# Optimization experiments

Hardware: AMD Instinct MI355X
Metric: run time of the kernel (lower is better)

Reference implementation:

```python
import jax, jax.numpy as jnp
import numpy as np

L, N = 200, 256  # event_list_length, num_nodes


def setup_inputs() -> dict:
    key = jax.random.key(0)
    ks = jax.random.split(key, 7)
    time = jax.random.uniform(ks[0], (2,), dtype=jnp.float32)
    event_list = jax.random.normal(ks[1], (L + 1, N, N), dtype=jnp.float32)
    u_begin = jax.random.uniform(ks[2], (N, N, 3), dtype=jnp.float32)
    # xavier-ish scales for params
    a = jax.random.normal(ks[3], (L, N, N, 3), dtype=jnp.float32) * 0.05
    w = jax.random.normal(ks[4], (L, N, 1, N), dtype=jnp.float32) * 0.05
    liner_w = jax.random.normal(ks[5], (N, 3), dtype=jnp.float32) * 0.5
    liner_b = jax.random.normal(ks[6], (N,), dtype=jnp.float32) * 0.1
    return {"time": time, "event_list": event_list, "u_begin": u_begin,
            "a": a, "w": w, "liner_w": liner_w, "liner_b": liner_b,
            "batch_size": 2}


def reference(time, event_list, u_begin, a, w, liner_w, liner_b, batch_size):
    # event_list[:-1]; consumed in pairs (start, start+1) with batch_size == 2
    T = event_list.shape[0] - 1
    S = T // batch_size                      # number of scan steps
    n = event_list.shape[1]
    e2 = event_list[:T].reshape(S, 2, n, n)          # [S,2,N,N]
    a2 = a[:T].reshape(S, 2, n, n, 3)                # [S,2,N,N,3]
    w2 = w[:T, :, 0, :].reshape(S, 2, n, n)          # [S,2,N,N] (squeeze the 1-dim)
    t0, t1 = time[0], time[1]                        # original always uses time[0], time[1]

    def step(u, xs):
        ep, ap, wp = xs                              # [2,N,N], [2,N,N,3], [2,N,N]
        # per-node scalar dot: w[start][node] @ event_begin[k][node]
        dot0 = jnp.einsum('nk,nk->n', wp[0], ep[0])  # [N]
        dot1 = jnp.einsum('nk,nk->n', wp[1], ep[1])
        # math.exp in the original returns a Python float -> constant w.r.t. autograd
        f0 = jax.lax.stop_gradient(jnp.exp(-dot0 * t0))[:, None, None]
        f1 = jax.lax.stop_gradient(jnp.exp(-dot1 * t1))[:, None, None]
        lamda = u + ap[0] * f0 + ap[1] * f1          # [N,N,3]
        temp = jax.nn.softmax(lamda, axis=-1)        # softmax over the 3-dim (dim=1 of [N,3] per node)
        # per-node Linear(3,1): temp[node] @ W_node^T + b_node -> [N,N]
        out = jnp.einsum('nmc,nc->nm', temp, liner_w) + liner_b[:, None]
        # state update was .detach().cpu().numpy() -> stop_gradient
        return jax.lax.stop_gradient(temp), out

    _, outs = jax.lax.scan(step, u_begin, (e2, a2, w2))
    return outs                                      # [S, N, N] == [T/2, N, N]
```

## Files before the change

### kernel.cpp

```cpp
#include <hip/hip_runtime.h>


#define NN    256
#define TT    200
#define SS    100
#define DRING 6

__global__ __launch_bounds__(256) void f_kernel(
    const float* __restrict__ timep,
    const float* __restrict__ ev,
    const float* __restrict__ w,
    float* __restrict__ fws)
{
    const int tid  = threadIdx.x;
    const int lane = tid & 63;
    const int row  = blockIdx.x * 4 + (tid >> 6);
    const int t    = row >> 8;
    const int n    = row & 255;

    const size_t off = (size_t)t * (NN * NN) + (size_t)n * NN;
    const float4 wv  = ((const float4*)(w  + off))[lane];
    const float4 evv = ((const float4*)(ev + off))[lane];

    float d = wv.x * evv.x;
    d = fmaf(wv.y, evv.y, d);
    d = fmaf(wv.z, evv.z, d);
    d = fmaf(wv.w, evv.w, d);
#pragma unroll
    for (int o = 1; o < 64; o <<= 1) d += __shfl_xor(d, o, 64);

    if (lane == 0) {
        const float tsel = (t & 1) ? timep[1] : timep[0];
        fws[n * TT + t] = __expf(-d * tsel);
    }
}

__global__ __launch_bounds__(256) void scan_kernel(
    const float* __restrict__ fws,
    const float* __restrict__ ub,
    const float* __restrict__ a,
    const float* __restrict__ lw,
    const float* __restrict__ lb,
    float* __restrict__ out)
{
    __shared__ float stg[DRING][4][768];
    __shared__ float fsl[TT];

    const int n    = blockIdx.x;
    const int tid  = threadIdx.x;
    const int lane = tid & 63;
    const int wv   = tid >> 6;

    if (tid < TT) fsl[tid] = fws[n * TT + tid];

    const size_t cb = (size_t)n * (NN * 3) + (size_t)tid * 3;
    float u0 = ub[cb + 0], u1 = ub[cb + 1], u2 = ub[cb + 2];
    const float w0 = lw[n * 3 + 0];
    const float w1 = lw[n * 3 + 1];
    const float w2 = lw[n * 3 + 2];
    const float bb = lb[n];

    const int m3 = tid * 3;
    float* op = out + (size_t)n * NN + tid;

    __syncthreads();

    const float* abase = a + (size_t)n * (NN * 3) + (size_t)lane * 4;

#define STAGE(qq, bidx)                                                        \
    do {                                                                       \
        const float* gp_ = abase + (size_t)(4 * (qq) + wv) * ((size_t)NN * NN * 3); \
        float* lp_ = &stg[bidx][wv][0];                                        \
        __builtin_amdgcn_global_load_lds(                                      \
            (const __attribute__((address_space(1))) void*)gp_,                \
            (__attribute__((address_space(3))) void*)lp_, 16, 0, 0);           \
        __builtin_amdgcn_global_load_lds(                                      \
            (const __attribute__((address_space(1))) void*)(gp_ + 256),        \
            (__attribute__((address_space(3))) void*)(lp_ + 256), 16, 0, 0);   \
        __builtin_amdgcn_global_load_lds(                                      \
            (const __attribute__((address_space(1))) void*)(gp_ + 512),        \
            (__attribute__((address_space(3))) void*)(lp_ + 512), 16, 0, 0);   \
    } while (0)

    STAGE(0, 0); STAGE(1, 1); STAGE(2, 2); STAGE(3, 3); STAGE(4, 4);

#define STEPX(BI, SA, SB, FA, FB, SOUT)                                        \
    do {                                                                       \
        float l0 = fmaf(stg[BI][SA][m3 + 0], FA, fmaf(stg[BI][SB][m3 + 0], FB, u0)); \
        float l1 = fmaf(stg[BI][SA][m3 + 1], FA, fmaf(stg[BI][SB][m3 + 1], FB, u1)); \
        float l2 = fmaf(stg[BI][SA][m3 + 2], FA, fmaf(stg[BI][SB][m3 + 2], FB, u2)); \
        float mx = fmaxf(l0, fmaxf(l1, l2));                                   \
        float e0 = __expf(l0 - mx), e1 = __expf(l1 - mx), e2 = __expf(l2 - mx);\
        float iv = __builtin_amdgcn_rcpf(e0 + e1 + e2);                        \
        u0 = e0 * iv; u1 = e1 * iv; u2 = e2 * iv;                              \
        __builtin_nontemporal_store(fmaf(u0, w0, fmaf(u1, w1, fmaf(u2, w2, bb))), \
                                    op + (size_t)(SOUT) * (NN * NN));          \
    } while (0)

#define PHASE(GG, VN, DOSTAGE, BI)                                             \
    do {                                                                       \
        asm volatile("s_waitcnt vmcnt(" #VN ")" ::: "memory");                 \
        __builtin_amdgcn_s_barrier();                                          \
        asm volatile("" ::: "memory");                                         \
        if (DOSTAGE) {                                                         \
            const int bs_ = (BI) ? (BI) - 1 : (DRING - 1);                     \
            STAGE((GG) + DRING - 1, bs_);                                      \
        }                                                                      \
        asm volatile("" ::: "memory");                                         \
        const float fa0 = fsl[4 * (GG) + 0], fb0 = fsl[4 * (GG) + 1];          \
        STEPX(BI, 0, 1, fa0, fb0, 2 * (GG));                                   \
        const float fa1 = fsl[4 * (GG) + 2], fb1 = fsl[4 * (GG) + 3];          \
        STEPX(BI, 2, 3, fa1, fb1, 2 * (GG) + 1);                               \
    } while (0)

    PHASE(0, 12, 1, 0);
    PHASE(1, 14, 1, 1);
    PHASE(2, 16, 1, 2);
    PHASE(3, 18, 1, 3);
    PHASE(4, 20, 1, 4);
    {
        int b = 5;
        for (int g = 5; g <= 44; ++g) {
            PHASE(g, 22, 1, b);
            b = (b == DRING - 1) ? 0 : b + 1;
        }
    }
    PHASE(45, 22, 0, 3);
    PHASE(46, 19, 0, 4);
    PHASE(47, 16, 0, 5);
    PHASE(48, 13, 0, 0);
    PHASE(49, 10, 0, 1);

#undef PHASE
#undef STEPX
#undef STAGE
}

extern "C" void kernel_launch(void* const* d_in, const int* in_sizes, int n_in,
                              void* d_out, int out_size, void* d_ws, size_t ws_size,
                              hipStream_t stream) {
    const float* timep = (const float*)d_in[0];
    const float* ev    = (const float*)d_in[1];
    const float* ub    = (const float*)d_in[2];
    const float* a     = (const float*)d_in[3];
    const float* w     = (const float*)d_in[4];
    const float* lw    = (const float*)d_in[5];
    const float* lb    = (const float*)d_in[6];
    float* out = (float*)d_out;
    float* fws = (float*)d_ws;

    f_kernel<<<(TT * NN) / 4, 256, 0, stream>>>(timep, ev, w, fws);
    scan_kernel<<<NN, 256, 0, stream>>>(fws, ub, a, lw, lb, out);
}
```

Measured before the change: 308.0 us.

## Fuse decay-factor computation into scan kernel and deepen LDS prefetch ring

Removes the separate f_kernel and computes each node's 200 exp-decay factors inside the scan block, writing them straight to shared memory while the first a-tiles are already being prefetched. This drops one launch and the workspace round trip. The async LDS ring grows from 6 to 8 stages, with vmcnt thresholds adjusted to match. The cost is that only 256 blocks now do the dot-product work serially inside the scan kernel, and more LDS is used per block.

```diff
diff --git a/kernel.cpp b/kernel.cpp
--- a/kernel.cpp
+++ b/kernel.cpp
@@ -4,41 +4,14 @@
 #define NN    256
 #define TT    200
 #define SS    100
-#define DRING 6
+#define DRING 8
 
-__global__ __launch_bounds__(256) void f_kernel(
+__global__ __launch_bounds__(256) void fused_kernel(
     const float* __restrict__ timep,
     const float* __restrict__ ev,
-    const float* __restrict__ w,
-    float* __restrict__ fws)
-{
-    const int tid  = threadIdx.x;
-    const int lane = tid & 63;
-    const int row  = blockIdx.x * 4 + (tid >> 6);
-    const int t    = row >> 8;
-    const int n    = row & 255;
-
-    const size_t off = (size_t)t * (NN * NN) + (size_t)n * NN;
-    const float4 wv  = ((const float4*)(w  + off))[lane];
-    const float4 evv = ((const float4*)(ev + off))[lane];
-
-    float d = wv.x * evv.x;
-    d = fmaf(wv.y, evv.y, d);
-    d = fmaf(wv.z, evv.z, d);
-    d = fmaf(wv.w, evv.w, d);
-#pragma unroll
-    for (int o = 1; o < 64; o <<= 1) d += __shfl_xor(d, o, 64);
-
-    if (lane == 0) {
-        const float tsel = (t & 1) ? timep[1] : timep[0];
-        fws[n * TT + t] = __expf(-d * tsel);
-    }
-}
-
-__global__ __launch_bounds__(256) void scan_kernel(
-    const float* __restrict__ fws,
     const float* __restrict__ ub,
     const float* __restrict__ a,
+    const float* __restrict__ w,
     const float* __restrict__ lw,
     const float* __restrict__ lb,
     float* __restrict__ out)
@@ -50,20 +23,6 @@
     const int tid  = threadIdx.x;
     const int lane = tid & 63;
     const int wv   = tid >> 6;
-
-    if (tid < TT) fsl[tid] = fws[n * TT + tid];
-
-    const size_t cb = (size_t)n * (NN * 3) + (size_t)tid * 3;
-    float u0 = ub[cb + 0], u1 = ub[cb + 1], u2 = ub[cb + 2];
-    const float w0 = lw[n * 3 + 0];
-    const float w1 = lw[n * 3 + 1];
-    const float w2 = lw[n * 3 + 2];
-    const float bb = lb[n];
-
-    const int m3 = tid * 3;
-    float* op = out + (size_t)n * NN + tid;
-
-    __syncthreads();
 
     const float* abase = a + (size_t)n * (NN * 3) + (size_t)lane * 4;
 
@@ -82,7 +41,52 @@
             (__attribute__((address_space(3))) void*)(lp_ + 512), 16, 0, 0);   \
     } while (0)
 
-    STAGE(0, 0); STAGE(1, 1); STAGE(2, 2); STAGE(3, 3); STAGE(4, 4);
+    STAGE(0, 0); STAGE(1, 1); STAGE(2, 2); STAGE(3, 3);
+    STAGE(4, 4); STAGE(5, 5); STAGE(6, 6);
+
+    {
+        const float t0 = timep[0];
+        const float t1 = timep[1];
+        const float tsel = (wv & 1) ? t1 : t0;
+        const size_t rowoff = (size_t)n * NN;
+        const float* wrow = w  + rowoff;
+        const float* erow = ev + rowoff;
+        for (int t = wv; t < TT; t += 20) {
+            float d[5];
+#pragma unroll
+            for (int q = 0; q < 5; ++q) {
+                const int tq = t + 4 * q;
+                float4 wvv = ((const float4*)(wrow + (size_t)tq * (NN * NN)))[lane];
+                float4 evv = ((const float4*)(erow + (size_t)tq * (NN * NN)))[lane];
+                float dq = wvv.x * evv.x;
+                dq = fmaf(wvv.y, evv.y, dq);
+                dq = fmaf(wvv.z, evv.z, dq);
+                dq = fmaf(wvv.w, evv.w, dq);
+                d[q] = dq;
+            }
+#pragma unroll
+            for (int o = 1; o < 64; o <<= 1) {
+#pragma unroll
+                for (int q = 0; q < 5; ++q) d[q] += __shfl_xor(d[q], o, 64);
+            }
+            if (lane == 0) {
+#pragma unroll
+                for (int q = 0; q < 5; ++q)
+                    fsl[t + 4 * q] = __expf(-d[q] * tsel);
+            }
+        }
+    }
+
+    const size_t cb = (size_t)n * (NN * 3) + (size_t)tid * 3;
+    float u0 = ub[cb + 0], u1 = ub[cb + 1], u2 = ub[cb + 2];
+    const float w0 = lw[n * 3 + 0];
+    const float w1 = lw[n * 3 + 1];
+    const float w2 = lw[n * 3 + 2];
+    const float bb = lb[n];
+    const int m3 = tid * 3;
+    float* op = out + (size_t)n * NN + tid;
+
+    __syncthreads();
 
 #define STEPX(BI, SA, SB, FA, FB, SOUT)                                        \
     do {                                                                       \
@@ -100,36 +104,40 @@
 #define PHASE(GG, VN, DOSTAGE, BI)                                             \
     do {                                                                       \
         asm volatile("s_waitcnt vmcnt(" #VN ")" ::: "memory");                 \
+        __builtin_amdgcn_sched_barrier(0);                                     \
         __builtin_amdgcn_s_barrier();                                          \
-        asm volatile("" ::: "memory");                                         \
         if (DOSTAGE) {                                                         \
             const int bs_ = (BI) ? (BI) - 1 : (DRING - 1);                     \
             STAGE((GG) + DRING - 1, bs_);                                      \
         }                                                                      \
-        asm volatile("" ::: "memory");                                         \
+        __builtin_amdgcn_sched_barrier(0);                                     \
         const float fa0 = fsl[4 * (GG) + 0], fb0 = fsl[4 * (GG) + 1];          \
         STEPX(BI, 0, 1, fa0, fb0, 2 * (GG));                                   \
         const float fa1 = fsl[4 * (GG) + 2], fb1 = fsl[4 * (GG) + 3];          \
         STEPX(BI, 2, 3, fa1, fb1, 2 * (GG) + 1);                               \
     } while (0)
 
-    PHASE(0, 12, 1, 0);
-    PHASE(1, 14, 1, 1);
-    PHASE(2, 16, 1, 2);
-    PHASE(3, 18, 1, 3);
-    PHASE(4, 20, 1, 4);
+    PHASE(0, 18, 1, 0);
+    PHASE(1, 20, 1, 1);
+    PHASE(2, 22, 1, 2);
+    PHASE(3, 24, 1, 3);
+    PHASE(4, 26, 1, 4);
+    PHASE(5, 28, 1, 5);
+    PHASE(6, 30, 1, 6);
     {
-        int b = 5;
-        for (int g = 5; g <= 44; ++g) {
-            PHASE(g, 22, 1, b);
-            b = (b == DRING - 1) ? 0 : b + 1;
+        int b = 7;
+        for (int g = 7; g <= 42; ++g) {
+            PHASE(g, 32, 1, b);
+            b = (b + 1) & 7;
         }
     }
-    PHASE(45, 22, 0, 3);
-    PHASE(46, 19, 0, 4);
-    PHASE(47, 16, 0, 5);
-    PHASE(48, 13, 0, 0);
-    PHASE(49, 10, 0, 1);
+    PHASE(43, 32, 0, 3);
+    PHASE(44, 29, 0, 4);
+    PHASE(45, 26, 0, 5);
+    PHASE(46, 23, 0, 6);
+    PHASE(47, 20, 0, 7);
+    PHASE(48, 17, 0, 0);
+    PHASE(49, 14, 0, 1);
 
 #undef PHASE
 #undef STEPX
@@ -147,8 +155,6 @@
     const float* lw    = (const float*)d_in[5];
     const float* lb    = (const float*)d_in[6];
     float* out = (float*)d_out;
-    float* fws = (float*)d_ws;
 
-    f_kernel<<<(TT * NN) / 4, 256, 0, stream>>>(timep, ev, w, fws);
-    scan_kernel<<<NN, 256, 0, stream>>>(fws, ub, a, lw, lb, out);
+    fused_kernel<<<NN, 256, 0, stream>>>(timep, ev, ub, a, w, lw, lb, out);
 }
```

New measurement: 309.3 us. No clear change (+0.4%).

## Fuse exponent-factor kernel into scan kernel with register prefetch ring

Applied to the files above, without the earlier changes.

Merges the per-row dot/exp kernel into the scan kernel, so each block computes its own node's decay factors in chunks, interleaved with the scan steps. This removes the second launch and the workspace round trip. The LDS staging ring for `a` is replaced by a per-thread register ring of eight steps loaded directly from global memory. In exchange, each block now also streams the w and ev rows for its node, and it adds more barriers and register pressure.

```diff
diff --git a/kernel.cpp b/kernel.cpp
--- a/kernel.cpp
+++ b/kernel.cpp
@@ -1,139 +1,160 @@
 #include <hip/hip_runtime.h>
 
 
-#define NN    256
-#define TT    200
-#define SS    100
-#define DRING 6
+#define NN 256
+#define TT 200
+#define SS 100
+#define RD 8
 
-__global__ __launch_bounds__(256) void f_kernel(
+__global__ __launch_bounds__(256) void fused_kernel(
     const float* __restrict__ timep,
     const float* __restrict__ ev,
-    const float* __restrict__ w,
-    float* __restrict__ fws)
-{
-    const int tid  = threadIdx.x;
-    const int lane = tid & 63;
-    const int row  = blockIdx.x * 4 + (tid >> 6);
-    const int t    = row >> 8;
-    const int n    = row & 255;
-
-    const size_t off = (size_t)t * (NN * NN) + (size_t)n * NN;
-    const float4 wv  = ((const float4*)(w  + off))[lane];
-    const float4 evv = ((const float4*)(ev + off))[lane];
-
-    float d = wv.x * evv.x;
-    d = fmaf(wv.y, evv.y, d);
-    d = fmaf(wv.z, evv.z, d);
-    d = fmaf(wv.w, evv.w, d);
-#pragma unroll
-    for (int o = 1; o < 64; o <<= 1) d += __shfl_xor(d, o, 64);
-
-    if (lane == 0) {
-        const float tsel = (t & 1) ? timep[1] : timep[0];
-        fws[n * TT + t] = __expf(-d * tsel);
-    }
-}
-
-__global__ __launch_bounds__(256) void scan_kernel(
-    const float* __restrict__ fws,
     const float* __restrict__ ub,
     const float* __restrict__ a,
+    const float* __restrict__ w,
     const float* __restrict__ lw,
     const float* __restrict__ lb,
     float* __restrict__ out)
 {
-    __shared__ float stg[DRING][4][768];
-    __shared__ float fsl[TT];
+    __shared__ float2 fs2[SS];
 
     const int n    = blockIdx.x;
     const int tid  = threadIdx.x;
     const int lane = tid & 63;
     const int wv   = tid >> 6;
 
-    if (tid < TT) fsl[tid] = fws[n * TT + tid];
+    const float tm0 = timep[0];
+    const float tm1 = timep[1];
 
+    const float* wrow = w  + (size_t)n * NN;
+    const float* erow = ev + (size_t)n * NN;
+
+    float4 wA, eA, wB, eB, wC, eC, wD, eD;
+
+#define LOADROWS(WX, EX, WY, EY, TB)                                           \
+    do {                                                                       \
+        const size_t r0_ = (size_t)(TB) * (NN * NN);                           \
+        WX = ((const float4*)(wrow + r0_))[lane];                              \
+        EX = ((const float4*)(erow + r0_))[lane];                              \
+        WY = ((const float4*)(wrow + r0_ + NN * NN))[lane];                    \
+        EY = ((const float4*)(erow + r0_ + NN * NN))[lane];                    \
+    } while (0)
+
+    LOADROWS(wA, eA, wB, eB, 2 * wv);
+
+    const size_t TS = (size_t)NN * NN * 3;
     const size_t cb = (size_t)n * (NN * 3) + (size_t)tid * 3;
+    const float* ab = a + cb;
+    float rg[RD][6];
+#pragma unroll
+    for (int j = 0; j < RD; ++j) {
+        const float* p_ = ab + (size_t)(2 * j) * TS;
+        rg[j][0] = p_[0];      rg[j][1] = p_[1];      rg[j][2] = p_[2];
+        rg[j][3] = p_[TS + 0]; rg[j][4] = p_[TS + 1]; rg[j][5] = p_[TS + 2];
+    }
+
     float u0 = ub[cb + 0], u1 = ub[cb + 1], u2 = ub[cb + 2];
     const float w0 = lw[n * 3 + 0];
     const float w1 = lw[n * 3 + 1];
     const float w2 = lw[n * 3 + 2];
     const float bb = lb[n];
-
-    const int m3 = tid * 3;
     float* op = out + (size_t)n * NN + tid;
 
-    __syncthreads();
-
-    const float* abase = a + (size_t)n * (NN * 3) + (size_t)lane * 4;
-
-#define STAGE(qq, bidx)                                                        \
+#define REDUCE(WX, EX, WY, EY, Q)                                              \
     do {                                                                       \
-        const float* gp_ = abase + (size_t)(4 * (qq) + wv) * ((size_t)NN * NN * 3); \
-        float* lp_ = &stg[bidx][wv][0];                                        \
-        __builtin_amdgcn_global_load_lds(                                      \
-            (const __attribute__((address_space(1))) void*)gp_,                \
-            (__attribute__((address_space(3))) void*)lp_, 16, 0, 0);           \
-        __builtin_amdgcn_global_load_lds(                                      \
-            (const __attribute__((address_space(1))) void*)(gp_ + 256),        \
-            (__attribute__((address_space(3))) void*)(lp_ + 256), 16, 0, 0);   \
-        __builtin_amdgcn_global_load_lds(                                      \
-            (const __attribute__((address_space(1))) void*)(gp_ + 512),        \
-            (__attribute__((address_space(3))) void*)(lp_ + 512), 16, 0, 0);   \
+        float d0_ = WX.x * EX.x;                                               \
+        d0_ = fmaf(WX.y, EX.y, d0_);                                           \
+        d0_ = fmaf(WX.z, EX.z, d0_);                                           \
+        d0_ = fmaf(WX.w, EX.w, d0_);                                           \
+        float d1_ = WY.x * EY.x;                                               \
+        d1_ = fmaf(WY.y, EY.y, d1_);                                           \
+        d1_ = fmaf(WY.z, EY.z, d1_);                                           \
+        d1_ = fmaf(WY.w, EY.w, d1_);                                           \
+        _Pragma("unroll")                                                      \
+        for (int o_ = 1; o_ < 64; o_ <<= 1) {                                  \
+            d0_ += __shfl_xor(d0_, o_, 64);                                    \
+            d1_ += __shfl_xor(d1_, o_, 64);                                    \
+        }                                                                      \
+        if (lane == 0)                                                         \
+            fs2[4 * (Q) + wv] =                                                \
+                make_float2(__expf(-d0_ * tm0), __expf(-d1_ * tm1));           \
     } while (0)
 
-    STAGE(0, 0); STAGE(1, 1); STAGE(2, 2); STAGE(3, 3); STAGE(4, 4);
-
-#define STEPX(BI, SA, SB, FA, FB, SOUT)                                        \
+#define FENCE_BAR                                                              \
     do {                                                                       \
-        float l0 = fmaf(stg[BI][SA][m3 + 0], FA, fmaf(stg[BI][SB][m3 + 0], FB, u0)); \
-        float l1 = fmaf(stg[BI][SA][m3 + 1], FA, fmaf(stg[BI][SB][m3 + 1], FB, u1)); \
-        float l2 = fmaf(stg[BI][SA][m3 + 2], FA, fmaf(stg[BI][SB][m3 + 2], FB, u2)); \
-        float mx = fmaxf(l0, fmaxf(l1, l2));                                   \
-        float e0 = __expf(l0 - mx), e1 = __expf(l1 - mx), e2 = __expf(l2 - mx);\
-        float iv = __builtin_amdgcn_rcpf(e0 + e1 + e2);                        \
-        u0 = e0 * iv; u1 = e1 * iv; u2 = e2 * iv;                              \
-        __builtin_nontemporal_store(fmaf(u0, w0, fmaf(u1, w1, fmaf(u2, w2, bb))), \
-                                    op + (size_t)(SOUT) * (NN * NN));          \
+        asm volatile("s_waitcnt lgkmcnt(0)" ::: "memory");                     \
+        __builtin_amdgcn_s_barrier();                                          \
+        __builtin_amdgcn_sched_barrier(0);                                     \
     } while (0)
 
-#define PHASE(GG, VN, DOSTAGE, BI)                                             \
+#define STEP(S, J, RF)                                                         \
     do {                                                                       \
-        asm volatile("s_waitcnt vmcnt(" #VN ")" ::: "memory");                 \
-        __builtin_amdgcn_s_barrier();                                          \
-        asm volatile("" ::: "memory");                                         \
-        if (DOSTAGE) {                                                         \
-            const int bs_ = (BI) ? (BI) - 1 : (DRING - 1);                     \
-            STAGE((GG) + DRING - 1, bs_);                                      \
+        const float2 ff_ = fs2[(S)];                                           \
+        float l0_ = fmaf(rg[J][0], ff_.x, fmaf(rg[J][3], ff_.y, u0));          \
+        float l1_ = fmaf(rg[J][1], ff_.x, fmaf(rg[J][4], ff_.y, u1));          \
+        float l2_ = fmaf(rg[J][2], ff_.x, fmaf(rg[J][5], ff_.y, u2));          \
+        if (RF) {           \
+            const float* pR_ = ab + (size_t)(2 * ((S) + RD)) * TS;             \
+            rg[J][0] = pR_[0];                                                 \
+            rg[J][1] = pR_[1];                                                 \
+            rg[J][2] = pR_[2];                                                 \
+            rg[J][3] = pR_[TS + 0];                                            \
+            rg[J][4] = pR_[TS + 1];                                            \
+            rg[J][5] = pR_[TS + 2];                                            \
         }                                                                      \
-        asm volatile("" ::: "memory");                                         \
-        const float fa0 = fsl[4 * (GG) + 0], fb0 = fsl[4 * (GG) + 1];          \
-        STEPX(BI, 0, 1, fa0, fb0, 2 * (GG));                                   \
-        const float fa1 = fsl[4 * (GG) + 2], fb1 = fsl[4 * (GG) + 3];          \
-        STEPX(BI, 2, 3, fa1, fb1, 2 * (GG) + 1);                               \
+        float mx_ = fmaxf(l0_, fmaxf(l1_, l2_));                               \
+        float e0_ = __expf(l0_ - mx_);                                         \
+        float e1_ = __expf(l1_ - mx_);                                         \
+        float e2_ = __expf(l2_ - mx_);                                         \
+        float iv_ = __builtin_amdgcn_rcpf(e0_ + e1_ + e2_);                    \
+        u0 = e0_ * iv_;                                                        \
+        u1 = e1_ * iv_;                                                        \
+        u2 = e2_ * iv_;                                                        \
+        __builtin_nontemporal_store(                                           \
+            fmaf(u0, w0, fmaf(u1, w1, fmaf(u2, w2, bb))),                      \
+            op + (size_t)(S) * (NN * NN));                                     \
     } while (0)
 
-    PHASE(0, 12, 1, 0);
-    PHASE(1, 14, 1, 1);
-    PHASE(2, 16, 1, 2);
-    PHASE(3, 18, 1, 3);
-    PHASE(4, 20, 1, 4);
-    {
-        int b = 5;
-        for (int g = 5; g <= 44; ++g) {
-            PHASE(g, 22, 1, b);
-            b = (b == DRING - 1) ? 0 : b + 1;
+    LOADROWS(wC, eC, wD, eD, 8 + 2 * wv);
+    REDUCE(wA, eA, wB, eB, 0);
+    FENCE_BAR;
+
+    for (int i = 1; i <= 12; ++i) {
+        const int qo = 2 * i - 1;
+        LOADROWS(wA, eA, wB, eB, 8 * (qo + 1) + 2 * wv);
+        REDUCE(wC, eC, wD, eD, qo);
+        FENCE_BAR;
+        {
+            const int s0 = 4 * (qo - 1);
+            STEP(s0 + 0, 0, 1);
+            STEP(s0 + 1, 1, 1);
+            STEP(s0 + 2, 2, 1);
+            STEP(s0 + 3, 3, 1);
+        }
+        const int qe  = 2 * i;
+        const int tnx = (qe < 24) ? (8 * (qe + 1)) : 0;
+        LOADROWS(wC, eC, wD, eD, tnx + 2 * wv);
+        REDUCE(wA, eA, wB, eB, qe);
+        FENCE_BAR;
+        {
+            const int s0 = 4 * (qe - 1);
+            const int rf = (qe != 24);
+            STEP(s0 + 0, 4, rf);
+            STEP(s0 + 1, 5, rf);
+            STEP(s0 + 2, 6, rf);
+            STEP(s0 + 3, 7, rf);
         }
     }
-    PHASE(45, 22, 0, 3);
-    PHASE(46, 19, 0, 4);
-    PHASE(47, 16, 0, 5);
-    PHASE(48, 13, 0, 0);
-    PHASE(49, 10, 0, 1);
 
-#undef PHASE
-#undef STEPX
-#undef STAGE
+    STEP(96, 0, 0);
+    STEP(97, 1, 0);
+    STEP(98, 2, 0);
+    STEP(99, 3, 0);
+
+#undef STEP
+#undef FENCE_BAR
+#undef REDUCE
+#undef LOADROWS
 }
 
 extern "C" void kernel_launch(void* const* d_in, const int* in_sizes, int n_in,
@@ -147,8 +168,6 @@
     const float* lw    = (const float*)d_in[5];
     const float* lb    = (const float*)d_in[6];
     float* out = (float*)d_out;
-    float* fws = (float*)d_ws;
 
-    f_kernel<<<(TT * NN) / 4, 256, 0, stream>>>(timep, ev, w, fws);
-    scan_kernel<<<NN, 256, 0, stream>>>(fws, ub, a, lw, lb, out);
+    fused_kernel<<<NN, 256, 0, stream>>>(timep, ev, ub, a, w, lw, lb, out);
 }
```

Measured after the change: 308.4 us. No clear change (+0.1%).
